# Optimization experiments

Measured on AMD Instinct MI355X. Metric: run time of the kernel, lower is better.

## Reference

```python
import jax, jax.numpy as jnp
import numpy as np

N = 100000   # nodes
F = 32       # input features
D = 64       # dim_inner
E = 1600000  # edges
G = 2000     # graphs
C = 10       # classes
L = 4        # GIN layers
BN_EPS = 1e-5


def _bn(h, gamma, beta):
    # training-mode BatchNorm1d over node axis (biased variance, as torch)
    mu = jnp.mean(h, axis=0)
    var = jnp.mean((h - mu) ** 2, axis=0)
    return gamma * (h - mu) * jax.lax.rsqrt(var + BN_EPS) + beta


def setup_inputs() -> dict:
    key = jax.random.key(0)
    ks = jax.random.split(key, 24)
    s = 0.05
    f32 = jnp.float32
    x = jax.random.normal(ks[0], (N, F), f32)
    edge_index = jax.random.randint(ks[1], (2, E), 0, N)
    batch_ids = jnp.sort(jax.random.randint(ks[2], (N,), 0, G))
    y = jax.random.randint(ks[3], (G,), 0, C)
    W_enc = jax.random.normal(ks[4], (F, D), f32) * s
    b_enc = jnp.zeros((D,), f32)
    W1 = jax.random.normal(ks[5], (L, D, D), f32) * s
    b1 = jnp.zeros((L, D), f32)
    g1 = jnp.ones((L, D), f32)
    be1 = jnp.zeros((L, D), f32)
    W2 = jax.random.normal(ks[6], (L, D, D), f32) * s
    b2 = jnp.zeros((L, D), f32)
    gout = jnp.ones((L, D), f32)
    bout = jnp.zeros((L, D), f32)
    fcW0 = jax.random.normal(ks[7], (F, C), f32) * s
    fcb0 = jnp.zeros((C,), f32)
    fcW = jax.random.normal(ks[8], (L, D, C), f32) * s
    fcb = jnp.zeros((L, C), f32)
    return dict(x=x, edge_index=edge_index, batch_ids=batch_ids, y=y,
                W_enc=W_enc, b_enc=b_enc, W1=W1, b1=b1, g1=g1, be1=be1,
                W2=W2, b2=b2, gout=gout, bout=bout,
                fcW0=fcW0, fcb0=fcb0, fcW=fcW, fcb=fcb)


def reference(x, edge_index, batch_ids, y, W_enc, b_enc, W1, b1, g1, be1,
              W2, b2, gout, bout, fcW0, fcb0, fcW, fcb):
    src, dst = edge_index[0], edge_index[1]
    h = x @ W_enc + b_enc  # x_encoder
    layer_outs = []
    for i in range(L):
        # GINConv, eps=0: (1+eps)*x + sum_{j->i} x_j  (scatter-add over edges)
        agg = jax.ops.segment_sum(h[src], dst, num_segments=N)
        m = h + agg
        m = jax.nn.relu(_bn(m @ W1[i] + b1[i], g1[i], be1[i]))  # MLP part 1
        m = m @ W2[i] + b2[i]                                    # MLP part 2
        h = jax.nn.relu(_bn(m, gout[i], bout[i]))                # outer BN+ReLU
        layer_outs.append(h)
    # jumping-knowledge: pooled raw features + each layer through its fc head
    out = jax.ops.segment_sum(x, batch_ids, num_segments=G) @ fcW0 + fcb0
    for i in range(L):
        pooled = jax.ops.segment_sum(layer_outs[i], batch_ids, num_segments=G)
        out = out + pooled @ fcW[i] + fcb[i]
    return (out, y)
```

## Files before the change

### kernel.cpp

```cpp
#include <hip/hip_runtime.h>


#define BN_EPS 1e-5f
#define CURS_STRIDE 16

typedef __attribute__((ext_vector_type(8))) short short8;
typedef __attribute__((ext_vector_type(4))) float f32x4;

__device__ __forceinline__ unsigned int pack_bf16x2(float a, float b) {
    unsigned int ua = __float_as_uint(a);
    unsigned int ub = __float_as_uint(b);
    ua = (ua + 0x7FFFu + ((ua >> 16) & 1u)) >> 16;
    ub = (ub + 0x7FFFu + ((ub >> 16) & 1u)) >> 16;
    return ua | (ub << 16);
}
__device__ __forceinline__ unsigned short bf16_1(float f) {
    unsigned int u = __float_as_uint(f);
    u = (u + 0x7FFFu + ((u >> 16) & 1u)) >> 16;
    return (unsigned short)u;
}
__device__ __forceinline__ float2 unpack_bf16x2(unsigned int u) {
    float2 r;
    r.x = __uint_as_float(u << 16);
    r.y = __uint_as_float(u & 0xFFFF0000u);
    return r;
}

template<bool BN>
__device__ __forceinline__ void acc_row8(float (&acc)[8], uint4 p,
                                         const float* sc, const float* sh) {
    unsigned int pp[4] = {p.x, p.y, p.z, p.w};
    #pragma unroll
    for (int t = 0; t < 4; t++) {
        float2 f = unpack_bf16x2(pp[t]);
        if (BN) {
            f.x = fmaxf(fmaf(f.x, sc[2 * t],     sh[2 * t]),     0.f);
            f.y = fmaxf(fmaf(f.y, sc[2 * t + 1], sh[2 * t + 1]), 0.f);
        }
        acc[2 * t]     += f.x;
        acc[2 * t + 1] += f.y;
    }
}

template<bool BN>
__global__ __launch_bounds__(256)
void gin_gemm1(const int* __restrict__ rowp, const int* __restrict__ srcs,
               const unsigned int* __restrict__ hb,
               const float* __restrict__ bsum, const float* __restrict__ bsumsq,
               const float* __restrict__ gamma, const float* __restrict__ beta,
               float invN,
               const float* __restrict__ W, const float* __restrict__ bias,
               unsigned short* __restrict__ out,
               float* __restrict__ stat_sum, float* __restrict__ stat_sumsq,
               int N)
{
    constexpr int AS = 72, WS = 72, KH = 2;
    __shared__ short a_lds[128 * AS];
    __shared__ short wt_lds[64 * WS];
    __shared__ float ssf[128];
    __shared__ float red[512];

    const int tid = threadIdx.x;
    const int nb  = blockIdx.x * 128;
    const int l   = tid & 63;
    const int w   = tid >> 6;
    const int ln  = l & 15;
    const int q   = l >> 4;

    if (BN) {
        if (tid < 64) {
            float mu  = bsum[tid] * invN;
            float var = bsumsq[tid] * invN - mu * mu;
            float s   = gamma[tid] * rsqrtf(var + BN_EPS);
            ssf[tid]      = s;
            ssf[64 + tid] = beta[tid] - s * mu;
        }
        __syncthreads();
    }

    for (int idx = tid; idx < 64 * 64; idx += 256) {
        int k = idx >> 6, n = idx & 63;
        wt_lds[n * WS + k] = (short)bf16_1(W[idx]);
    }

    const uint4* hb4 = (const uint4*)hb;
    const int cc = tid & 7;
    const int rl = tid >> 3;
    float sc[8], sh[8];
    if (BN) {
        #pragma unroll
        for (int j = 0; j < 8; j++) {
            sc[j] = ssf[cc * 8 + j];
            sh[j] = ssf[64 + cc * 8 + j];
        }
    }
    for (int it = 0; it < 4; it++) {
        int rloc = it * 32 + rl;
        int n = nb + rloc;
        float acc[8] = {0.f, 0.f, 0.f, 0.f, 0.f, 0.f, 0.f, 0.f};
        if (n < N) {
            uint4 p = hb4[(size_t)n * 8 + cc];
            acc_row8<BN>(acc, p, sc, sh);
            int e = rowp[n], end = rowp[n + 1];
            for (; e + 3 < end; e += 4) {
                int a0 = srcs[e], a1 = srcs[e + 1], a2 = srcs[e + 2], a3 = srcs[e + 3];
                uint4 p0 = hb4[(size_t)a0 * 8 + cc];
                uint4 p1 = hb4[(size_t)a1 * 8 + cc];
                uint4 p2 = hb4[(size_t)a2 * 8 + cc];
                uint4 p3 = hb4[(size_t)a3 * 8 + cc];
                acc_row8<BN>(acc, p0, sc, sh);
                acc_row8<BN>(acc, p1, sc, sh);
                acc_row8<BN>(acc, p2, sc, sh);
                acc_row8<BN>(acc, p3, sc, sh);
            }
            for (; e < end; e++) {
                uint4 pp = hb4[(size_t)srcs[e] * 8 + cc];
                acc_row8<BN>(acc, pp, sc, sh);
            }
        }
        uint4 o;
        o.x = pack_bf16x2(acc[0], acc[1]);
        o.y = pack_bf16x2(acc[2], acc[3]);
        o.z = pack_bf16x2(acc[4], acc[5]);
        o.w = pack_bf16x2(acc[6], acc[7]);
        *(uint4*)&a_lds[rloc * AS + cc * 8] = o;
    }
    __syncthreads();

    short8 afrag[2][KH], bfrag[4][KH];
    const int rw = w * 32;
    #pragma unroll
    for (int mt = 0; mt < 2; mt++)
        #pragma unroll
        for (int kh = 0; kh < KH; kh++)
            afrag[mt][kh] = *(const short8*)&a_lds[(rw + mt * 16 + ln) * AS + kh * 32 + q * 8];
    #pragma unroll
    for (int nt = 0; nt < 4; nt++)
        #pragma unroll
        for (int kh = 0; kh < KH; kh++)
            bfrag[nt][kh] = *(const short8*)&wt_lds[(nt * 16 + ln) * WS + kh * 32 + q * 8];

    f32x4 acc[2][4];
    #pragma unroll
    for (int nt = 0; nt < 4; nt++) {
        float bv = bias[nt * 16 + ln];
        #pragma unroll
        for (int mt = 0; mt < 2; mt++)
            acc[mt][nt] = (f32x4){bv, bv, bv, bv};
    }
    #pragma unroll
    for (int kh = 0; kh < KH; kh++)
        #pragma unroll
        for (int mt = 0; mt < 2; mt++)
            #pragma unroll
            for (int nt = 0; nt < 4; nt++)
                acc[mt][nt] = __builtin_amdgcn_mfma_f32_16x16x32_bf16(
                    afrag[mt][kh], bfrag[nt][kh], acc[mt][nt], 0, 0, 0);

    #pragma unroll
    for (int mt = 0; mt < 2; mt++)
        #pragma unroll
        for (int reg = 0; reg < 4; reg++) {
            int row = nb + rw + mt * 16 + q * 4 + reg;
            if (row < N)
                #pragma unroll
                for (int nt = 0; nt < 4; nt++)
                    out[(size_t)row * 64 + nt * 16 + ln] = bf16_1(acc[mt][nt][reg]);
        }

    {
        float s1[4] = {0.f, 0.f, 0.f, 0.f};
        float s2[4] = {0.f, 0.f, 0.f, 0.f};
        #pragma unroll
        for (int mt = 0; mt < 2; mt++)
            #pragma unroll
            for (int reg = 0; reg < 4; reg++) {
                int row = nb + rw + mt * 16 + q * 4 + reg;
                if (row < N)
                    #pragma unroll
                    for (int nt = 0; nt < 4; nt++) {
                        float v = acc[mt][nt][reg];
                        s1[nt] += v;
                        s2[nt] += v * v;
                    }
            }
        #pragma unroll
        for (int nt = 0; nt < 4; nt++) {
            s1[nt] += __shfl_xor(s1[nt], 16);
            s1[nt] += __shfl_xor(s1[nt], 32);
            s2[nt] += __shfl_xor(s2[nt], 16);
            s2[nt] += __shfl_xor(s2[nt], 32);
        }
        __syncthreads();
        if (l < 16) {
            #pragma unroll
            for (int nt = 0; nt < 4; nt++) {
                red[w * 64 + nt * 16 + l]       = s1[nt];
                red[256 + w * 64 + nt * 16 + l] = s2[nt];
            }
        }
        __syncthreads();
        if (tid < 64) {
            float t1 = red[tid] + red[64 + tid] + red[128 + tid] + red[192 + tid];
            float t2 = red[256 + tid] + red[320 + tid] + red[384 + tid] + red[448 + tid];
            unsafeAtomicAdd(&stat_sum[tid],   t1);
            unsafeAtomicAdd(&stat_sumsq[tid], t2);
        }
    }
}

template<int K, int INK, bool STATS>
__global__ __launch_bounds__(256)
void mfma_gemm(const void* __restrict__ Av,
               const float* __restrict__ bn_sum, const float* __restrict__ bn_sumsq,
               const float* __restrict__ gamma, const float* __restrict__ beta,
               float invN,
               const float* __restrict__ W, const float* __restrict__ bias,
               unsigned short* __restrict__ out,
               float* __restrict__ stat_sum, float* __restrict__ stat_sumsq,
               int N)
{
    constexpr int AS  = K + 8;
    constexpr int WS  = K + 8;
    constexpr int CPR = K / 8;
    constexpr int KH  = K / 32;

    __shared__ short a_lds[128 * AS];
    __shared__ short wt_lds[64 * WS];
    __shared__ float ssf[128];
    __shared__ float red[512];

    const int tid = threadIdx.x;
    const int nb  = blockIdx.x * 128;
    const int l   = tid & 63;
    const int w   = tid >> 6;
    const int ln  = l & 15;
    const int q   = l >> 4;

    if (INK == 2) {
        if (tid < 64) {
            float mu  = bn_sum[tid] * invN;
            float var = bn_sumsq[tid] * invN - mu * mu;
            float s   = gamma[tid] * rsqrtf(var + BN_EPS);
            ssf[tid]      = s;
            ssf[64 + tid] = beta[tid] - s * mu;
        }
        __syncthreads();
    }

    for (int idx = tid; idx < K * 64; idx += 256) {
        int k = idx >> 6, n = idx & 63;
        wt_lds[n * WS + k] = (short)bf16_1(W[idx]);
    }

    for (int c = tid; c < 128 * CPR; c += 256) {
        int rloc = c / CPR;
        int j    = c % CPR;
        int row  = nb + rloc;
        uint4 p = make_uint4(0u, 0u, 0u, 0u);
        if (row < N) {
            if (INK == 1) {
                const float4* xr = (const float4*)Av;
                float4 f0 = xr[(size_t)row * (K / 4) + 2 * j];
                float4 f1 = xr[(size_t)row * (K / 4) + 2 * j + 1];
                p.x = pack_bf16x2(f0.x, f0.y); p.y = pack_bf16x2(f0.z, f0.w);
                p.z = pack_bf16x2(f1.x, f1.y); p.w = pack_bf16x2(f1.z, f1.w);
            } else {
                p = ((const uint4*)Av)[(size_t)row * CPR + j];
                if (INK == 2) {
                    int k0 = j * 8;
                    unsigned int* pp = (unsigned int*)&p;
                    #pragma unroll
                    for (int t = 0; t < 4; t++) {
                        float2 f = unpack_bf16x2(pp[t]);
                        int k = k0 + 2 * t;
                        f.x = fmaxf(fmaf(f.x, ssf[k],     ssf[64 + k]),     0.f);
                        f.y = fmaxf(fmaf(f.y, ssf[k + 1], ssf[64 + k + 1]), 0.f);
                        pp[t] = pack_bf16x2(f.x, f.y);
                    }
                }
            }
        }
        *(uint4*)&a_lds[rloc * AS + j * 8] = p;
    }
    __syncthreads();

    short8 afrag[2][KH], bfrag[4][KH];
    const int rw = w * 32;
    #pragma unroll
    for (int mt = 0; mt < 2; mt++)
        #pragma unroll
        for (int kh = 0; kh < KH; kh++)
            afrag[mt][kh] = *(const short8*)&a_lds[(rw + mt * 16 + ln) * AS + kh * 32 + q * 8];
    #pragma unroll
    for (int nt = 0; nt < 4; nt++)
        #pragma unroll
        for (int kh = 0; kh < KH; kh++)
            bfrag[nt][kh] = *(const short8*)&wt_lds[(nt * 16 + ln) * WS + kh * 32 + q * 8];

    f32x4 acc[2][4];
    #pragma unroll
    for (int nt = 0; nt < 4; nt++) {
        float bv = bias[nt * 16 + ln];
        #pragma unroll
        for (int mt = 0; mt < 2; mt++)
            acc[mt][nt] = (f32x4){bv, bv, bv, bv};
    }
    #pragma unroll
    for (int kh = 0; kh < KH; kh++)
        #pragma unroll
        for (int mt = 0; mt < 2; mt++)
            #pragma unroll
            for (int nt = 0; nt < 4; nt++)
                acc[mt][nt] = __builtin_amdgcn_mfma_f32_16x16x32_bf16(
                    afrag[mt][kh], bfrag[nt][kh], acc[mt][nt], 0, 0, 0);

    #pragma unroll
    for (int mt = 0; mt < 2; mt++)
        #pragma unroll
        for (int reg = 0; reg < 4; reg++) {
            int row = nb + rw + mt * 16 + q * 4 + reg;
            if (row < N)
                #pragma unroll
                for (int nt = 0; nt < 4; nt++)
                    out[(size_t)row * 64 + nt * 16 + ln] = bf16_1(acc[mt][nt][reg]);
        }

    if (STATS) {
        float s1[4] = {0.f, 0.f, 0.f, 0.f};
        float s2[4] = {0.f, 0.f, 0.f, 0.f};
        #pragma unroll
        for (int mt = 0; mt < 2; mt++)
            #pragma unroll
            for (int reg = 0; reg < 4; reg++) {
                int row = nb + rw + mt * 16 + q * 4 + reg;
                if (row < N)
                    #pragma unroll
                    for (int nt = 0; nt < 4; nt++) {
                        float v = acc[mt][nt][reg];
                        s1[nt] += v;
                        s2[nt] += v * v;
                    }
            }
        #pragma unroll
        for (int nt = 0; nt < 4; nt++) {
            s1[nt] += __shfl_xor(s1[nt], 16);
            s1[nt] += __shfl_xor(s1[nt], 32);
            s2[nt] += __shfl_xor(s2[nt], 16);
            s2[nt] += __shfl_xor(s2[nt], 32);
        }
        __syncthreads();
        if (l < 16) {
            #pragma unroll
            for (int nt = 0; nt < 4; nt++) {
                red[w * 64 + nt * 16 + l]       = s1[nt];
                red[256 + w * 64 + nt * 16 + l] = s2[nt];
            }
        }
        __syncthreads();
        if (tid < 64) {
            float t1 = red[tid] + red[64 + tid] + red[128 + tid] + red[192 + tid];
            float t2 = red[256 + tid] + red[320 + tid] + red[384 + tid] + red[448 + tid];
            unsafeAtomicAdd(&stat_sum[tid],   t1);
            unsafeAtomicAdd(&stat_sumsq[tid], t2);
        }
    }
}

__global__ __launch_bounds__(256)
void bucket_hist(const int* __restrict__ dst, int* __restrict__ bhist,
                 int E, int nb)
{
    __shared__ int lh[1024];
    for (int i = threadIdx.x; i < 1024; i += 256) lh[i] = 0;
    __syncthreads();
    for (int e = blockIdx.x * 256 + threadIdx.x; e < E; e += gridDim.x * 256)
        atomicAdd(&lh[dst[e] >> 7], 1);
    __syncthreads();
    for (int i = threadIdx.x; i < nb; i += 256)
        if (lh[i]) atomicAdd(&bhist[i], lh[i]);
}

__global__ __launch_bounds__(1024)
void bucket_scan(const int* __restrict__ bhist, int* __restrict__ bbase,
                 int* __restrict__ bcur, int nb)
{
    __shared__ int sm[1024];
    int t = threadIdx.x;
    int v = (t < nb) ? bhist[t] : 0;
    sm[t] = v; __syncthreads();
    for (int off = 1; off < 1024; off <<= 1) {
        int add = (t >= off) ? sm[t - off] : 0;
        __syncthreads();
        sm[t] += add;
        __syncthreads();
    }
    if (t <= nb) {
        int ex = sm[t] - v;
        bbase[t] = ex;
        if (t < nb) bcur[t * CURS_STRIDE] = ex;
    }
}

__global__ __launch_bounds__(256)
void bucket_scatter(const int* __restrict__ src, const int* __restrict__ dst,
                    int* __restrict__ bcur, int* __restrict__ ebuf,
                    int E, int nb)
{
    constexpr int CH = 4096;
    __shared__ int            key[CH];
    __shared__ unsigned short bid[CH];
    __shared__ int lh[800];
    __shared__ int lbase[800];

    const int t    = threadIdx.x;
    const int base = blockIdx.x * CH;
    const int cnt  = min(CH, E - base);

    for (int i = t; i < nb; i += 256) lh[i] = 0;
    __syncthreads();

    for (int i = t; i < cnt; i += 256) {
        int d = dst[base + i];
        int s = src[base + i];
        int b = d >> 7;
        key[i] = (s << 7) | (d & 127);
        bid[i] = (unsigned short)b;
        atomicAdd(&lh[b], 1);
    }
    __syncthreads();

    for (int i = t; i < nb; i += 256) {
        int c = lh[i];
        if (c) lbase[i] = atomicAdd(&bcur[i * CURS_STRIDE], c);
        lh[i] = 0;
    }
    __syncthreads();

    for (int i = t; i < cnt; i += 256) {
        int b = bid[i];
        int p = atomicAdd(&lh[b], 1);
        ebuf[lbase[b] + p] = key[i];
    }
}

__global__ __launch_bounds__(256)
void bucket_csr(const int* __restrict__ bbase, const int* __restrict__ ebuf,
                int* __restrict__ row, int* __restrict__ srcs, int N, int E)
{
    __shared__ int lh[128], lofs[128], lcur[128];
    const int b   = blockIdx.x;
    const int tid = threadIdx.x;
    const int beg = bbase[b], end = bbase[b + 1];

    if (tid < 128) lh[tid] = 0;
    __syncthreads();
    for (int e = beg + tid; e < end; e += 256)
        atomicAdd(&lh[ebuf[e] & 127], 1);
    __syncthreads();

    int v = (tid < 128) ? lh[tid] : 0;
    if (tid < 128) lofs[tid] = v;
    __syncthreads();
    for (int off = 1; off < 128; off <<= 1) {
        int add = 0;
        if (tid < 128 && tid >= off) add = lofs[tid - off];
        __syncthreads();
        if (tid < 128) lofs[tid] += add;
        __syncthreads();
    }
    if (tid < 128) {
        int ex = lofs[tid] - v;
        lcur[tid] = ex;
        int node = b * 128 + tid;
        if (node < N) row[node] = beg + ex;
    }
    if (b == 0 && tid == 0) row[N] = E;
    __syncthreads();

    for (int e = beg + tid; e < end; e += 256) {
        int pk = ebuf[e];
        int p = atomicAdd(&lcur[pk & 127], 1);
        srcs[beg + p] = pk >> 7;
    }
}

__global__ __launch_bounds__(256)
void pool_nodes(const unsigned short* __restrict__ hb,
                const float* __restrict__ bsum, const float* __restrict__ bsumsq,
                const float* __restrict__ gamma, const float* __restrict__ beta,
                float invN, const int* __restrict__ batch,
                float* __restrict__ pooled, int N)
{
    int d  = threadIdx.x & 63;
    int nl = threadIdx.x >> 6;
    int nb = blockIdx.x * 32;
    float mu  = bsum[d] * invN;
    float var = bsumsq[d] * invN - mu * mu;
    float s   = gamma[d] * rsqrtf(var + BN_EPS);
    float sh  = beta[d] - s * mu;
    float acc = 0.f;
    int cg = -1;
    #pragma unroll
    for (int r = 0; r < 8; r++) {
        int n = nb + nl * 8 + r;
        if (n >= N) break;
        int g = batch[n];
        if (g != cg) {
            if (cg >= 0) unsafeAtomicAdd(&pooled[(size_t)cg * 64 + d], acc);
            acc = 0.f; cg = g;
        }
        float v = __uint_as_float(((unsigned int)hb[(size_t)n * 64 + d]) << 16);
        acc += fmaxf(fmaf(v, s, sh), 0.f);
    }
    if (cg >= 0) unsafeAtomicAdd(&pooled[(size_t)cg * 64 + d], acc);
}

__global__ __launch_bounds__(256)
void pool_x(const float* __restrict__ x, const int* __restrict__ batch,
            float* __restrict__ px, int N)
{
    int f  = threadIdx.x & 31;
    int nl = threadIdx.x >> 5;
    int nb = blockIdx.x * 64;
    float acc = 0.f;
    int cg = -1;
    #pragma unroll
    for (int r = 0; r < 8; r++) {
        int n = nb + nl * 8 + r;
        if (n >= N) break;
        int g = batch[n];
        if (g != cg) {
            if (cg >= 0) unsafeAtomicAdd(&px[(size_t)cg * 32 + f], acc);
            acc = 0.f; cg = g;
        }
        acc += x[(size_t)n * 32 + f];
    }
    if (cg >= 0) unsafeAtomicAdd(&px[(size_t)cg * 32 + f], acc);
}

__global__ __launch_bounds__(256)
void head_kernel(const float* __restrict__ px, const float* __restrict__ pl,
                 const float* __restrict__ fcW0, const float* __restrict__ fcb0,
                 const float* __restrict__ fcW, const float* __restrict__ fcb,
                 const int* __restrict__ y, float* __restrict__ out, int G)
{
    int tid = blockIdx.x * 256 + threadIdx.x;
    int total = G * 10;
    if (tid < total) {
        int g = tid / 10, c = tid % 10;
        float acc = fcb0[c];
        const float* pxg = px + (size_t)g * 32;
        #pragma unroll
        for (int k = 0; k < 32; k++) acc = fmaf(pxg[k], fcW0[k * 10 + c], acc);
        #pragma unroll
        for (int i = 0; i < 4; i++) {
            acc += fcb[i * 10 + c];
            const float* pg = pl + ((size_t)i * G + g) * 64;
            const float* w  = fcW + i * 640;
            #pragma unroll
            for (int k = 0; k < 64; k++) acc = fmaf(pg[k], w[k * 10 + c], acc);
        }
        out[tid] = acc;
    } else if (tid < total + G) {
        out[tid] = (float)y[tid - total];
    }
}

extern "C" void kernel_launch(void* const* d_in, const int* in_sizes, int n_in,
                              void* d_out, int out_size, void* d_ws, size_t ws_size,
                              hipStream_t stream)
{
    const float* x     = (const float*)d_in[0];
    const int*   ei    = (const int*)  d_in[1];
    const int*   batch = (const int*)  d_in[2];
    const int*   y     = (const int*)  d_in[3];
    const float* W_enc = (const float*)d_in[4];
    const float* b_enc = (const float*)d_in[5];
    const float* W1    = (const float*)d_in[6];
    const float* b1    = (const float*)d_in[7];
    const float* g1    = (const float*)d_in[8];
    const float* be1   = (const float*)d_in[9];
    const float* W2    = (const float*)d_in[10];
    const float* b2    = (const float*)d_in[11];
    const float* gout  = (const float*)d_in[12];
    const float* bout  = (const float*)d_in[13];
    const float* fcW0  = (const float*)d_in[14];
    const float* fcb0  = (const float*)d_in[15];
    const float* fcW   = (const float*)d_in[16];
    const float* fcb   = (const float*)d_in[17];

    const int N = in_sizes[0] / 32;
    const int E = in_sizes[1] / 2;
    const int G = in_sizes[3];
    const int* src = ei;
    const int* dst = ei + E;
    const int NB = (N + 127) / 128;

    unsigned int* m  = (unsigned int*)d_ws;
    unsigned int* hb = m + (size_t)N * 32;
    float* stats = (float*)(hb + (size_t)N * 32);
    float* px    = stats + 1024;
    float* pl    = px + (size_t)G * 32;
    int*   row   = (int*)(pl + (size_t)4 * G * 64);
    int*   srcs  = row + (N + 1);
    int*   mi    = (int*)m;
    int*   bhist = mi;
    int*   bbase = mi + 1024;
    int*   bcur  = mi + 2048;
    int*   ebuf  = mi + 2048 + 800 * CURS_STRIDE;

    size_t zbytes = (size_t)(1024 + G * 32 + 4 * G * 64) * sizeof(float);
    hipMemsetAsync(stats, 0, zbytes, stream);
    hipMemsetAsync(bhist, 0, 1024 * sizeof(int), stream);

    bucket_hist<<<160, 256, 0, stream>>>(dst, bhist, E, NB);
    bucket_scan<<<1, 1024, 0, stream>>>(bhist, bbase, bcur, NB);
    bucket_scatter<<<(E + 4095) / 4096, 256, 0, stream>>>(src, dst, bcur, ebuf, E, NB);
    bucket_csr<<<NB, 256, 0, stream>>>(bbase, ebuf, row, srcs, N, E);

    const int gb = (N + 127) / 128;
    const float invN = 1.0f / (float)N;

    mfma_gemm<32, 1, false><<<gb, 256, 0, stream>>>(
        x, nullptr, nullptr, nullptr, nullptr, 0.f,
        W_enc, b_enc, (unsigned short*)hb, nullptr, nullptr, N);
    pool_x<<<(N + 63) / 64, 256, 0, stream>>>(x, batch, px, N);

    for (int i = 0; i < 4; i++) {
        float* s1a = stats + (i * 2 + 0) * 128;
        float* s1b = s1a + 64;
        float* s2a = stats + (i * 2 + 1) * 128;
        float* s2b = s2a + 64;

        if (i == 0) {
            gin_gemm1<false><<<gb, 256, 0, stream>>>(
                row, srcs, hb, nullptr, nullptr, nullptr, nullptr, 0.f,
                W1 + (size_t)i * 4096, b1 + i * 64, (unsigned short*)m, s1a, s1b, N);
        } else {
            float* p2a = stats + ((i - 1) * 2 + 1) * 128;
            float* p2b = p2a + 64;
            gin_gemm1<true><<<gb, 256, 0, stream>>>(
                row, srcs, hb, p2a, p2b,
                gout + (i - 1) * 64, bout + (i - 1) * 64, invN,
                W1 + (size_t)i * 4096, b1 + i * 64, (unsigned short*)m, s1a, s1b, N);
        }

        mfma_gemm<64, 2, true><<<gb, 256, 0, stream>>>(
            m, s1a, s1b, g1 + i * 64, be1 + i * 64, invN,
            W2 + (size_t)i * 4096, b2 + i * 64, (unsigned short*)hb, s2a, s2b, N);

        pool_nodes<<<(N + 31) / 32, 256, 0, stream>>>(
            (const unsigned short*)hb, s2a, s2b, gout + i * 64, bout + i * 64, invN,
            batch, pl + (size_t)i * G * 64, N);
    }

    head_kernel<<<(G * 10 + G + 255) / 256, 256, 0, stream>>>(
        px, pl, fcW0, fcb0, fcW, fcb, y, (float*)d_out, G);
}
```

Before: 564.6 us.

## Apply outer BN+ReLU once in pool kernel, write back normalized features

The pooling kernel now applies the outer BatchNorm+ReLU, writes the normalized bf16 features back into hb, and pools them. The next layer's gather no longer re-applies BN to every gathered neighbor row, which removes per-edge FMA/max work. The gather loop is also unrolled to 8 independent loads to raise memory-level parallelism. The cost is an extra write of hb per layer, plus the pool kernel now runs on the critical path before the next gather.

```diff
diff --git a/kernel.cpp b/kernel.cpp
--- a/kernel.cpp
+++ b/kernel.cpp
@@ -26,29 +26,19 @@
     return r;
 }
 
-template<bool BN>
-__device__ __forceinline__ void acc_row8(float (&acc)[8], uint4 p,
-                                         const float* sc, const float* sh) {
+__device__ __forceinline__ void acc_row8(float (&acc)[8], uint4 p) {
     unsigned int pp[4] = {p.x, p.y, p.z, p.w};
     #pragma unroll
     for (int t = 0; t < 4; t++) {
         float2 f = unpack_bf16x2(pp[t]);
-        if (BN) {
-            f.x = fmaxf(fmaf(f.x, sc[2 * t],     sh[2 * t]),     0.f);
-            f.y = fmaxf(fmaf(f.y, sc[2 * t + 1], sh[2 * t + 1]), 0.f);
-        }
         acc[2 * t]     += f.x;
         acc[2 * t + 1] += f.y;
     }
 }
 
-template<bool BN>
 __global__ __launch_bounds__(256)
 void gin_gemm1(const int* __restrict__ rowp, const int* __restrict__ srcs,
                const unsigned int* __restrict__ hb,
-               const float* __restrict__ bsum, const float* __restrict__ bsumsq,
-               const float* __restrict__ gamma, const float* __restrict__ beta,
-               float invN,
                const float* __restrict__ W, const float* __restrict__ bias,
                unsigned short* __restrict__ out,
                float* __restrict__ stat_sum, float* __restrict__ stat_sumsq,
@@ -57,7 +47,6 @@
     constexpr int AS = 72, WS = 72, KH = 2;
     __shared__ short a_lds[128 * AS];
     __shared__ short wt_lds[64 * WS];
-    __shared__ float ssf[128];
     __shared__ float red[512];
 
     const int tid = threadIdx.x;
@@ -67,17 +56,6 @@
     const int ln  = l & 15;
     const int q   = l >> 4;
 
-    if (BN) {
-        if (tid < 64) {
-            float mu  = bsum[tid] * invN;
-            float var = bsumsq[tid] * invN - mu * mu;
-            float s   = gamma[tid] * rsqrtf(var + BN_EPS);
-            ssf[tid]      = s;
-            ssf[64 + tid] = beta[tid] - s * mu;
-        }
-        __syncthreads();
-    }
-
     for (int idx = tid; idx < 64 * 64; idx += 256) {
         int k = idx >> 6, n = idx & 63;
         wt_lds[n * WS + k] = (short)bf16_1(W[idx]);
@@ -86,37 +64,30 @@
     const uint4* hb4 = (const uint4*)hb;
     const int cc = tid & 7;
     const int rl = tid >> 3;
-    float sc[8], sh[8];
-    if (BN) {
-        #pragma unroll
-        for (int j = 0; j < 8; j++) {
-            sc[j] = ssf[cc * 8 + j];
-            sh[j] = ssf[64 + cc * 8 + j];
-        }
-    }
     for (int it = 0; it < 4; it++) {
         int rloc = it * 32 + rl;
         int n = nb + rloc;
         float acc[8] = {0.f, 0.f, 0.f, 0.f, 0.f, 0.f, 0.f, 0.f};
         if (n < N) {
-            uint4 p = hb4[(size_t)n * 8 + cc];
-            acc_row8<BN>(acc, p, sc, sh);
+            acc_row8(acc, hb4[(size_t)n * 8 + cc]);
             int e = rowp[n], end = rowp[n + 1];
-            for (; e + 3 < end; e += 4) {
-                int a0 = srcs[e], a1 = srcs[e + 1], a2 = srcs[e + 2], a3 = srcs[e + 3];
-                uint4 p0 = hb4[(size_t)a0 * 8 + cc];
-                uint4 p1 = hb4[(size_t)a1 * 8 + cc];
-                uint4 p2 = hb4[(size_t)a2 * 8 + cc];
-                uint4 p3 = hb4[(size_t)a3 * 8 + cc];
-                acc_row8<BN>(acc, p0, sc, sh);
-                acc_row8<BN>(acc, p1, sc, sh);
-                acc_row8<BN>(acc, p2, sc, sh);
-                acc_row8<BN>(acc, p3, sc, sh);
-            }
-            for (; e < end; e++) {
-                uint4 pp = hb4[(size_t)srcs[e] * 8 + cc];
-                acc_row8<BN>(acc, pp, sc, sh);
-            }
+            for (; e + 7 < end; e += 8) {
+                uint4 p[8];
+                #pragma unroll
+                for (int j = 0; j < 8; j++)
+                    p[j] = hb4[(size_t)srcs[e + j] * 8 + cc];
+                #pragma unroll
+                for (int j = 0; j < 8; j++)
+                    acc_row8(acc, p[j]);
+            }
+            for (; e + 1 < end; e += 2) {
+                uint4 p0 = hb4[(size_t)srcs[e] * 8 + cc];
+                uint4 p1 = hb4[(size_t)srcs[e + 1] * 8 + cc];
+                acc_row8(acc, p0);
+                acc_row8(acc, p1);
+            }
+            if (e < end)
+                acc_row8(acc, hb4[(size_t)srcs[e] * 8 + cc]);
         }
         uint4 o;
         o.x = pack_bf16x2(acc[0], acc[1]);
@@ -486,20 +457,21 @@
 }
 
 __global__ __launch_bounds__(256)
-void pool_nodes(const unsigned short* __restrict__ hb,
-                const float* __restrict__ bsum, const float* __restrict__ bsumsq,
-                const float* __restrict__ gamma, const float* __restrict__ beta,
-                float invN, const int* __restrict__ batch,
-                float* __restrict__ pooled, int N)
-{
-    int d  = threadIdx.x & 63;
-    int nl = threadIdx.x >> 6;
-    int nb = blockIdx.x * 32;
-    float mu  = bsum[d] * invN;
-    float var = bsumsq[d] * invN - mu * mu;
-    float s   = gamma[d] * rsqrtf(var + BN_EPS);
-    float sh  = beta[d] - s * mu;
-    float acc = 0.f;
+void bn_pool(unsigned int* __restrict__ hb,
+             const float* __restrict__ bsum, const float* __restrict__ bsumsq,
+             const float* __restrict__ gamma, const float* __restrict__ beta,
+             float invN, const int* __restrict__ batch,
+             float* __restrict__ pooled, int N)
+{
+    int d2 = threadIdx.x & 31;
+    int nl = threadIdx.x >> 5;
+    int nb = blockIdx.x * 64;
+    int c0 = 2 * d2, c1 = c0 + 1;
+    float mu0 = bsum[c0] * invN, mu1 = bsum[c1] * invN;
+    float s0 = gamma[c0] * rsqrtf(bsumsq[c0] * invN - mu0 * mu0 + BN_EPS);
+    float s1 = gamma[c1] * rsqrtf(bsumsq[c1] * invN - mu1 * mu1 + BN_EPS);
+    float h0 = beta[c0] - s0 * mu0, h1 = beta[c1] - s1 * mu1;
+    float a0 = 0.f, a1 = 0.f;
     int cg = -1;
     #pragma unroll
     for (int r = 0; r < 8; r++) {
@@ -507,13 +479,23 @@
         if (n >= N) break;
         int g = batch[n];
         if (g != cg) {
-            if (cg >= 0) unsafeAtomicAdd(&pooled[(size_t)cg * 64 + d], acc);
-            acc = 0.f; cg = g;
-        }
-        float v = __uint_as_float(((unsigned int)hb[(size_t)n * 64 + d]) << 16);
-        acc += fmaxf(fmaf(v, s, sh), 0.f);
-    }
-    if (cg >= 0) unsafeAtomicAdd(&pooled[(size_t)cg * 64 + d], acc);
+            if (cg >= 0) {
+                unsafeAtomicAdd(&pooled[(size_t)cg * 64 + c0], a0);
+                unsafeAtomicAdd(&pooled[(size_t)cg * 64 + c1], a1);
+            }
+            a0 = a1 = 0.f; cg = g;
+        }
+        unsigned int u = hb[(size_t)n * 32 + d2];
+        float2 f = unpack_bf16x2(u);
+        f.x = fmaxf(fmaf(f.x, s0, h0), 0.f);
+        f.y = fmaxf(fmaf(f.y, s1, h1), 0.f);
+        hb[(size_t)n * 32 + d2] = pack_bf16x2(f.x, f.y);
+        a0 += f.x; a1 += f.y;
+    }
+    if (cg >= 0) {
+        unsafeAtomicAdd(&pooled[(size_t)cg * 64 + c0], a0);
+        unsafeAtomicAdd(&pooled[(size_t)cg * 64 + c1], a1);
+    }
 }
 
 __global__ __launch_bounds__(256)
@@ -619,7 +601,7 @@
     bucket_scatter<<<(E + 4095) / 4096, 256, 0, stream>>>(src, dst, bcur, ebuf, E, NB);
     bucket_csr<<<NB, 256, 0, stream>>>(bbase, ebuf, row, srcs, N, E);
 
-    const int gb = (N + 127) / 128;
+    const int gb = NB;
     const float invN = 1.0f / (float)N;
 
     mfma_gemm<32, 1, false><<<gb, 256, 0, stream>>>(
@@ -633,25 +615,16 @@
         float* s2a = stats + (i * 2 + 1) * 128;
         float* s2b = s2a + 64;
 
-        if (i == 0) {
-            gin_gemm1<false><<<gb, 256, 0, stream>>>(
-                row, srcs, hb, nullptr, nullptr, nullptr, nullptr, 0.f,
-                W1 + (size_t)i * 4096, b1 + i * 64, (unsigned short*)m, s1a, s1b, N);
-        } else {
-            float* p2a = stats + ((i - 1) * 2 + 1) * 128;
-            float* p2b = p2a + 64;
-            gin_gemm1<true><<<gb, 256, 0, stream>>>(
-                row, srcs, hb, p2a, p2b,
-                gout + (i - 1) * 64, bout + (i - 1) * 64, invN,
-                W1 + (size_t)i * 4096, b1 + i * 64, (unsigned short*)m, s1a, s1b, N);
-        }
+        gin_gemm1<<<gb, 256, 0, stream>>>(
+            row, srcs, hb, W1 + (size_t)i * 4096, b1 + i * 64,
+            (unsigned short*)m, s1a, s1b, N);
 
         mfma_gemm<64, 2, true><<<gb, 256, 0, stream>>>(
             m, s1a, s1b, g1 + i * 64, be1 + i * 64, invN,
             W2 + (size_t)i * 4096, b2 + i * 64, (unsigned short*)hb, s2a, s2b, N);
 
-        pool_nodes<<<(N + 31) / 32, 256, 0, stream>>>(
-            (const unsigned short*)hb, s2a, s2b, gout + i * 64, bout + i * 64, invN,
+        bn_pool<<<(N + 63) / 64, 256, 0, stream>>>(
+            hb, s2a, s2b, gout + i * 64, bout + i * 64, invN,
             batch, pl + (size_t)i * G * 64, N);
     }
 
```

Result: slower. 634.3 us (+12.3%).
